# Kernel tuning notes

Measured on AMD Instinct MI355X. Metric: run time of the kernel, lower is better.

Reference implementation:

```python
import jax, jax.numpy as jnp
import numpy as np

KERNEL = 3
EPS = 1e-8
MIN_DENOM = 1e-6


def _entropy_map(x):
    # x: [B, C, H, W]. Zero-pad (matches nn.Unfold padding) and gather the
    # K = KERNEL**2 shifted views -> [B, C, K, H, W]. Window positions are
    # row-major (kh outer, kw inner), matching Unfold's channel-major layout
    # after view(B, C, K, H*W).
    B, C, H, W = x.shape
    p = KERNEL // 2
    xp = jnp.pad(x, ((0, 0), (0, 0), (p, p), (p, p)))
    patches = jnp.stack(
        [xp[:, :, i:i + H, j:j + W] for i in range(KERNEL) for j in range(KERNEL)],
        axis=2,
    )  # [B, C, K, H, W]
    prob = jax.nn.softmax(patches, axis=2) + EPS
    entropy = -jnp.sum(prob * jnp.log(prob), axis=2)  # [B, C, H, W]
    return entropy.mean(axis=1, keepdims=True)        # [B, 1, H, W]


def setup_inputs() -> dict:
    key = jax.random.key(0)
    x = jax.random.normal(key, (4, 64, 256, 256), dtype=jnp.float32)
    return {"x": x}


def reference(x) -> jnp.ndarray:
    e = _entropy_map(x)  # [B, 1, H, W]
    e_det = jax.lax.stop_gradient(e)
    e_min = e_det.min(axis=(1, 2, 3), keepdims=True)
    e_max = e_det.max(axis=(1, 2, 3), keepdims=True)
    denom = jnp.maximum(e_max - e_min, MIN_DENOM)
    return (e - e_min) / denom
```

## Files before the change

kernel.cpp:

```cpp
#include <hip/hip_runtime.h>
#include <math.h>

constexpr int Bb = 4, Cc = 64, Hh = 256, Ww = 256;
constexpr int RR = 4;
constexpr int CS = 4;
constexpr int NSTRIP = Hh / RR;
constexpr int NPX = Bb * Hh * Ww;
constexpr int NPX4 = NPX / 4;

#define LOG2E 1.44269504088896340736f
#define LN2   0.69314718055994530942f

__device__ __forceinline__ unsigned int fenc(float f) {
  unsigned int u = __float_as_uint(f);
  return (u & 0x80000000u) ? ~u : (u | 0x80000000u);
}
__device__ __forceinline__ float fdec(unsigned int k) {
  return __uint_as_float((k & 0x80000000u) ? (k ^ 0x80000000u) : ~k);
}

template <int DST>
__global__ __launch_bounds__(512) void entropy_kernel(const float* __restrict__ x,
                                                      float* __restrict__ out) {
  const int bx = blockIdx.x;
  const int cs = bx & 3;
  const int strip = (bx >> 2) & (NSTRIP - 1);
  const int b = bx >> 8;
  const int r0 = strip * RR;
  const int tx = threadIdx.x;
  const int ty = threadIdx.y;
  const int w0 = tx * 4;

  const size_t planeStride = (size_t)Hh * Ww;
  const float* xb = x + ((size_t)b * Cc + cs * 16 + ty * 2) * planeStride + w0;

  float acc[RR][4];
#pragma unroll
  for (int o = 0; o < RR; ++o)
#pragma unroll
    for (int i = 0; i < 4; ++i) acc[o][i] = 0.f;

#pragma unroll 1
  for (int cc = 0; cc < 2; ++cc) {
    const float* plane = xb + (size_t)cc * planeStride;

    float4 v[RR + 2];
#pragma unroll
    for (int j = 0; j < RR + 2; ++j) {
      const int row = r0 - 1 + j;
      if (row >= 0 && row < Hh)
        v[j] = *reinterpret_cast<const float4*>(plane + (size_t)row * Ww);
      else
        v[j] = make_float4(0.f, 0.f, 0.f, 0.f);
    }

    float ha[3][4], hb[3][4];
#pragma unroll
    for (int j = 0; j < RR + 2; ++j) {
      const float* vp = &v[j].x;
      float a[4], bb4[4];
#pragma unroll
      for (int i = 0; i < 4; ++i) {
        float t = __builtin_amdgcn_exp2f(vp[i] * LOG2E);
        a[i] = t;
        bb4[i] = vp[i] * t;
      }
      float la = __shfl_up(a[3], 1, 64);
      float lb = __shfl_up(bb4[3], 1, 64);
      float ra = __shfl_down(a[0], 1, 64);
      float rb = __shfl_down(bb4[0], 1, 64);
      la = (tx == 0) ? 1.f : la;   lb = (tx == 0) ? 0.f : lb;
      ra = (tx == 63) ? 1.f : ra;  rb = (tx == 63) ? 0.f : rb;
      const int s0 = j % 3;
      ha[s0][0] = la + a[0] + a[1];
      ha[s0][1] = a[0] + a[1] + a[2];
      ha[s0][2] = a[1] + a[2] + a[3];
      ha[s0][3] = a[2] + a[3] + ra;
      hb[s0][0] = lb + bb4[0] + bb4[1];
      hb[s0][1] = bb4[0] + bb4[1] + bb4[2];
      hb[s0][2] = bb4[1] + bb4[2] + bb4[3];
      hb[s0][3] = bb4[2] + bb4[3] + rb;
      if (j >= 2) {
        const int orow = j - 2;
#pragma unroll
        for (int i = 0; i < 4; ++i) {
          float s = ha[0][i] + ha[1][i] + ha[2][i];
          float w = hb[0][i] + hb[1][i] + hb[2][i];
          acc[orow][i] += LN2 * __builtin_amdgcn_logf(s) -
                          w * __builtin_amdgcn_rcpf(s);
        }
      }
    }
  }

  __shared__ float red[8][RR][4][64];
#pragma unroll
  for (int o = 0; o < RR; ++o)
#pragma unroll
    for (int i = 0; i < 4; ++i) red[ty][o][i][tx] = acc[o][i];
  __syncthreads();
  if (ty < RR) {
    const int o = ty;
    const size_t px = (size_t)(b * Hh + r0 + o) * Ww + w0;
    float vsum[4];
#pragma unroll
    for (int i = 0; i < 4; ++i) {
      float t = 0.f;
#pragma unroll
      for (int g = 0; g < 8; ++g) t += red[g][o][i][tx];
      vsum[i] = t;
    }
    if (DST == 0) {
      *reinterpret_cast<float4*>(out + (size_t)cs * NPX + px) =
          make_float4(vsum[0], vsum[1], vsum[2], vsum[3]);
    } else {
#pragma unroll
      for (int i = 0; i < 4; ++i) atomicAdd(out + px + i, vsum[i]);
    }
  }
}

__global__ __launch_bounds__(256) void combine_minmax(const float* __restrict__ pw,
                                                      float* __restrict__ e,
                                                      float* __restrict__ pm) {
  const int t = blockIdx.x * 256 + threadIdx.x;
  float4 v0 = reinterpret_cast<const float4*>(pw)[t];
  float4 v1 = reinterpret_cast<const float4*>(pw + NPX)[t];
  float4 v2 = reinterpret_cast<const float4*>(pw + 2 * (size_t)NPX)[t];
  float4 v3 = reinterpret_cast<const float4*>(pw + 3 * (size_t)NPX)[t];
  float4 v = make_float4(v0.x + v1.x + v2.x + v3.x, v0.y + v1.y + v2.y + v3.y,
                         v0.z + v1.z + v2.z + v3.z, v0.w + v1.w + v2.w + v3.w);
  reinterpret_cast<float4*>(e)[t] = v;

  float mn = fminf(fminf(v.x, v.y), fminf(v.z, v.w));
  float mx = fmaxf(fmaxf(v.x, v.y), fmaxf(v.z, v.w));
#pragma unroll
  for (int off = 32; off > 0; off >>= 1) {
    mn = fminf(mn, __shfl_down(mn, off, 64));
    mx = fmaxf(mx, __shfl_down(mx, off, 64));
  }
  __shared__ float smn[4], smx[4];
  const int wave = threadIdx.x >> 6;
  if ((threadIdx.x & 63) == 0) { smn[wave] = mn; smx[wave] = mx; }
  __syncthreads();
  if (threadIdx.x == 0) {
    pm[blockIdx.x]       = fminf(fminf(smn[0], smn[1]), fminf(smn[2], smn[3]));
    pm[256 + blockIdx.x] = fmaxf(fmaxf(smx[0], smx[1]), fmaxf(smx[2], smx[3]));
  }
}

__global__ __launch_bounds__(256) void norm_ws(float* __restrict__ e,
                                               const float* __restrict__ pm) {
  const int b = blockIdx.x >> 6;
  const int lane = threadIdx.x & 63;
  float mn = pm[b * 64 + lane];
  float mx = pm[256 + b * 64 + lane];
#pragma unroll
  for (int off = 32; off > 0; off >>= 1) {
    mn = fminf(mn, __shfl_down(mn, off, 64));
    mx = fmaxf(mx, __shfl_down(mx, off, 64));
  }
  mn = __shfl(mn, 0, 64);
  mx = __shfl(mx, 0, 64);
  const float inv = 1.0f / fmaxf(mx - mn, 1e-6f);

  const int t = blockIdx.x * 256 + threadIdx.x;
  float4 v = reinterpret_cast<float4*>(e)[t];
  v.x = (v.x - mn) * inv;
  v.y = (v.y - mn) * inv;
  v.z = (v.z - mn) * inv;
  v.w = (v.w - mn) * inv;
  reinterpret_cast<float4*>(e)[t] = v;
}

__global__ __launch_bounds__(256) void minmax_atomic(const float* __restrict__ e,
                                                     unsigned int* __restrict__ stats) {
  const int bx = blockIdx.x;
  const int b = bx >> 6;
  const float4 v = reinterpret_cast<const float4*>(
      e + (size_t)b * Hh * Ww + (bx & 63) * 1024)[threadIdx.x];
  float mn = fminf(fminf(v.x, v.y), fminf(v.z, v.w));
  float mx = fmaxf(fmaxf(v.x, v.y), fmaxf(v.z, v.w));
#pragma unroll
  for (int off = 32; off > 0; off >>= 1) {
    mn = fminf(mn, __shfl_down(mn, off, 64));
    mx = fmaxf(mx, __shfl_down(mx, off, 64));
  }
  __shared__ float smn[4], smx[4];
  const int wave = threadIdx.x >> 6;
  if ((threadIdx.x & 63) == 0) { smn[wave] = mn; smx[wave] = mx; }
  __syncthreads();
  if (threadIdx.x == 0) {
    atomicMin(&stats[b], fenc(fminf(fminf(smn[0], smn[1]), fminf(smn[2], smn[3]))));
    atomicMax(&stats[4 + b], fenc(fmaxf(fmaxf(smx[0], smx[1]), fmaxf(smx[2], smx[3]))));
  }
}

__global__ __launch_bounds__(256) void norm_atomic(float* __restrict__ e,
                                                   const unsigned int* __restrict__ stats) {
  const int t = blockIdx.x * 256 + threadIdx.x;
  const int b = t >> 14;
  const float mn = fdec(stats[b]);
  const float mx = fdec(stats[4 + b]);
  const float inv = 1.0f / fmaxf(mx - mn, 1e-6f);
  float4 v = reinterpret_cast<float4*>(e)[t];
  v.x = (v.x - mn) * inv;
  v.y = (v.y - mn) * inv;
  v.z = (v.z - mn) * inv;
  v.w = (v.w - mn) * inv;
  reinterpret_cast<float4*>(e)[t] = v;
}

extern "C" void kernel_launch(void* const* d_in, const int* in_sizes, int n_in,
                              void* d_out, int out_size, void* d_ws, size_t ws_size,
                              hipStream_t stream) {
  const float* x = (const float*)d_in[0];
  float* out = (float*)d_out;

  const size_t ws_needed = ((size_t)CS * NPX + 512) * sizeof(float);
  if (ws_size >= ws_needed) {
    float* pw = (float*)d_ws;
    float* pm = pw + (size_t)CS * NPX;
    entropy_kernel<0><<<dim3(Bb * NSTRIP * CS), dim3(64, 8), 0, stream>>>(x, pw);
    combine_minmax<<<dim3(NPX4 / 256), dim3(256), 0, stream>>>(pw, out, pm);
    norm_ws<<<dim3(NPX4 / 256), dim3(256), 0, stream>>>(out, pm);
  } else {
    unsigned int* stats = (unsigned int*)d_ws;
    hipMemsetAsync(out, 0, (size_t)NPX * sizeof(float), stream);
    hipMemsetAsync(stats, 0xFF, 4 * sizeof(unsigned int), stream);
    hipMemsetAsync(stats + 4, 0x00, 4 * sizeof(unsigned int), stream);
    entropy_kernel<1><<<dim3(Bb * NSTRIP * CS), dim3(64, 8), 0, stream>>>(x, out);
    minmax_atomic<<<dim3(Bb * 64), dim3(256), 0, stream>>>(out, stats);
    norm_atomic<<<dim3(NPX4 / 256), dim3(256), 0, stream>>>(out, stats);
  }
}
```

Baseline: 28.07 us.

## Fuse combine, min/max reduction and normalization into one kernel via last-block sync

Merges the combine_minmax and norm_ws kernels into a single finish_kernel. Each block keeps its summed entropy values in registers, publishes a partial min/max, and the last block per batch (found with an atomic counter) reduces the partials and sets a flag. All blocks spin on that flag before normalizing and writing out. This removes one kernel launch and the write-then-reread of the intermediate entropy map. The price is a spin-wait that relies on all 256 blocks being resident at the same time, and the counters are reset inside the entropy kernel.

```diff
diff --git a/kernel.cpp b/kernel.cpp
--- a/kernel.cpp
+++ b/kernel.cpp
@@ -21,8 +21,12 @@
 
 template <int DST>
 __global__ __launch_bounds__(512) void entropy_kernel(const float* __restrict__ x,
-                                                      float* __restrict__ out) {
+                                                      float* __restrict__ out,
+                                                      unsigned int* __restrict__ sync) {
   const int bx = blockIdx.x;
+  if (DST == 0 && bx == 0 && threadIdx.x < 8 && threadIdx.y == 0)
+    sync[threadIdx.x] = 0u;
+
   const int cs = bx & 3;
   const int strip = (bx >> 2) & (NSTRIP - 1);
   const int b = bx >> 8;
@@ -120,17 +124,21 @@
   }
 }
 
-__global__ __launch_bounds__(256) void combine_minmax(const float* __restrict__ pw,
-                                                      float* __restrict__ e,
-                                                      float* __restrict__ pm) {
-  const int t = blockIdx.x * 256 + threadIdx.x;
+__global__ __launch_bounds__(256) void finish_kernel(const float* __restrict__ pw,
+                                                     float* __restrict__ e,
+                                                     float* __restrict__ pm,
+                                                     float* __restrict__ stats,
+                                                     unsigned int* __restrict__ sync) {
+  const int bx = blockIdx.x;
+  const int b = bx >> 6;
+  const int t = bx * 256 + threadIdx.x;
+
   float4 v0 = reinterpret_cast<const float4*>(pw)[t];
-  float4 v1 = reinterpret_cast<const float4*>(pw + NPX)[t];
+  float4 v1 = reinterpret_cast<const float4*>(pw + (size_t)NPX)[t];
   float4 v2 = reinterpret_cast<const float4*>(pw + 2 * (size_t)NPX)[t];
   float4 v3 = reinterpret_cast<const float4*>(pw + 3 * (size_t)NPX)[t];
   float4 v = make_float4(v0.x + v1.x + v2.x + v3.x, v0.y + v1.y + v2.y + v3.y,
                          v0.z + v1.z + v2.z + v3.z, v0.w + v1.w + v2.w + v3.w);
-  reinterpret_cast<float4*>(e)[t] = v;
 
   float mn = fminf(fminf(v.x, v.y), fminf(v.z, v.w));
   float mx = fmaxf(fmaxf(v.x, v.y), fmaxf(v.z, v.w));
@@ -140,36 +148,49 @@
     mx = fmaxf(mx, __shfl_down(mx, off, 64));
   }
   __shared__ float smn[4], smx[4];
+  __shared__ int is_last;
   const int wave = threadIdx.x >> 6;
   if ((threadIdx.x & 63) == 0) { smn[wave] = mn; smx[wave] = mx; }
   __syncthreads();
   if (threadIdx.x == 0) {
-    pm[blockIdx.x]       = fminf(fminf(smn[0], smn[1]), fminf(smn[2], smn[3]));
-    pm[256 + blockIdx.x] = fmaxf(fmaxf(smx[0], smx[1]), fmaxf(smx[2], smx[3]));
-  }
-}
-
-__global__ __launch_bounds__(256) void norm_ws(float* __restrict__ e,
-                                               const float* __restrict__ pm) {
-  const int b = blockIdx.x >> 6;
-  const int lane = threadIdx.x & 63;
-  float mn = pm[b * 64 + lane];
-  float mx = pm[256 + b * 64 + lane];
-#pragma unroll
-  for (int off = 32; off > 0; off >>= 1) {
-    mn = fminf(mn, __shfl_down(mn, off, 64));
-    mx = fmaxf(mx, __shfl_down(mx, off, 64));
-  }
-  mn = __shfl(mn, 0, 64);
-  mx = __shfl(mx, 0, 64);
-  const float inv = 1.0f / fmaxf(mx - mn, 1e-6f);
-
-  const int t = blockIdx.x * 256 + threadIdx.x;
-  float4 v = reinterpret_cast<float4*>(e)[t];
-  v.x = (v.x - mn) * inv;
-  v.y = (v.y - mn) * inv;
-  v.z = (v.z - mn) * inv;
-  v.w = (v.w - mn) * inv;
+    pm[bx]       = fminf(fminf(smn[0], smn[1]), fminf(smn[2], smn[3]));
+    pm[256 + bx] = fmaxf(fmaxf(smx[0], smx[1]), fmaxf(smx[2], smx[3]));
+    __threadfence();
+    is_last = (atomicAdd(&sync[b], 1u) == 63u);
+  }
+  __syncthreads();
+  if (is_last && threadIdx.x < 64) {
+    __threadfence();
+    float rmn = pm[b * 64 + threadIdx.x];
+    float rmx = pm[256 + b * 64 + threadIdx.x];
+#pragma unroll
+    for (int off = 32; off > 0; off >>= 1) {
+      rmn = fminf(rmn, __shfl_down(rmn, off, 64));
+      rmx = fmaxf(rmx, __shfl_down(rmx, off, 64));
+    }
+    if (threadIdx.x == 0) {
+      stats[2 * b] = rmn;
+      stats[2 * b + 1] = 1.0f / fmaxf(rmx - rmn, 1e-6f);
+      __threadfence();
+      atomicExch(&sync[4 + b], 1u);
+    }
+  }
+
+  __shared__ float s_mn, s_inv;
+  if (threadIdx.x == 0) {
+    while (__hip_atomic_load(&sync[4 + b], __ATOMIC_ACQUIRE,
+                             __HIP_MEMORY_SCOPE_AGENT) == 0u) {
+      __builtin_amdgcn_s_sleep(2);
+    }
+    s_mn = stats[2 * b];
+    s_inv = stats[2 * b + 1];
+  }
+  __syncthreads();
+  const float mnb = s_mn, inv = s_inv;
+  v.x = (v.x - mnb) * inv;
+  v.y = (v.y - mnb) * inv;
+  v.z = (v.z - mnb) * inv;
+  v.w = (v.w - mnb) * inv;
   reinterpret_cast<float4*>(e)[t] = v;
 }
 
@@ -217,19 +238,20 @@
   const float* x = (const float*)d_in[0];
   float* out = (float*)d_out;
 
-  const size_t ws_needed = ((size_t)CS * NPX + 512) * sizeof(float);
+  const size_t ws_needed = ((size_t)CS * NPX + 512 + 8 + 8) * sizeof(float);
   if (ws_size >= ws_needed) {
     float* pw = (float*)d_ws;
     float* pm = pw + (size_t)CS * NPX;
-    entropy_kernel<0><<<dim3(Bb * NSTRIP * CS), dim3(64, 8), 0, stream>>>(x, pw);
-    combine_minmax<<<dim3(NPX4 / 256), dim3(256), 0, stream>>>(pw, out, pm);
-    norm_ws<<<dim3(NPX4 / 256), dim3(256), 0, stream>>>(out, pm);
+    float* stats = pm + 512;
+    unsigned int* sync = (unsigned int*)(stats + 8);
+    entropy_kernel<0><<<dim3(Bb * NSTRIP * CS), dim3(64, 8), 0, stream>>>(x, pw, sync);
+    finish_kernel<<<dim3(NPX4 / 256), dim3(256), 0, stream>>>(pw, out, pm, stats, sync);
   } else {
     unsigned int* stats = (unsigned int*)d_ws;
     hipMemsetAsync(out, 0, (size_t)NPX * sizeof(float), stream);
     hipMemsetAsync(stats, 0xFF, 4 * sizeof(unsigned int), stream);
     hipMemsetAsync(stats + 4, 0x00, 4 * sizeof(unsigned int), stream);
-    entropy_kernel<1><<<dim3(Bb * NSTRIP * CS), dim3(64, 8), 0, stream>>>(x, out);
+    entropy_kernel<1><<<dim3(Bb * NSTRIP * CS), dim3(64, 8), 0, stream>>>(x, out, nullptr);
     minmax_atomic<<<dim3(Bb * 64), dim3(256), 0, stream>>>(out, stats);
     norm_atomic<<<dim3(NPX4 / 256), dim3(256), 0, stream>>>(out, stats);
   }
```

Result: slower. 41.74 us (+48.7%).
